# Optimization experiments

Hardware: AMD Instinct MI355X
Metric: run time of the kernel (lower is better)

## Reference

```python
import jax, jax.numpy as jnp
import numpy as np

EMBED_DIM = 1024
NUM_HEADS = 16
HEAD_DIM = EMBED_DIM // NUM_HEADS


def setup_inputs() -> dict:
    key = jax.random.key(0)
    ks = jax.random.split(key, 9)
    B, S, D = 1, 4096, EMBED_DIM
    scale = 1.0 / np.sqrt(D)
    x = jax.random.normal(ks[0], (B, S, D), dtype=jnp.float32)
    # Linear weights stored as [in, out]; torch nn.Linear init ~ U(-1/sqrt(in), 1/sqrt(in))
    wq = jax.random.uniform(ks[1], (D, D), jnp.float32, -scale, scale)
    bq = jax.random.uniform(ks[2], (D,), jnp.float32, -scale, scale)
    wk = jax.random.uniform(ks[3], (D, D), jnp.float32, -scale, scale)
    bk = jax.random.uniform(ks[4], (D,), jnp.float32, -scale, scale)
    wv = jax.random.uniform(ks[5], (D, D), jnp.float32, -scale, scale)
    bv = jax.random.uniform(ks[6], (D,), jnp.float32, -scale, scale)
    wo = jax.random.uniform(ks[7], (D, D), jnp.float32, -scale, scale)
    bo = jax.random.uniform(ks[8], (D,), jnp.float32, -scale, scale)
    return {"x": x, "wq": wq, "bq": bq, "wk": wk, "bk": bk,
            "wv": wv, "bv": bv, "wo": wo, "bo": bo}


def reference(x, wq, bq, wk, bk, wv, bv, wo, bo):
    B, S, D = x.shape
    H, Hd = NUM_HEADS, HEAD_DIM
    # QKV projections
    q = x @ wq + bq  # [B,S,D]
    k = x @ wk + bk
    v = x @ wv + bv
    # split heads -> [B,H,S,Hd]
    q = q.reshape(B, S, H, Hd).transpose(0, 2, 1, 3)
    k = k.reshape(B, S, H, Hd).transpose(0, 2, 1, 3)
    v = v.reshape(B, S, H, Hd).transpose(0, 2, 1, 3)
    inv_sqrt_d = 1.0 / np.sqrt(Hd).astype(np.float32)
    scores = jnp.einsum('bhqd,bhkd->bhqk', q, k) * inv_sqrt_d  # [B,H,S,S]
    attn = jax.nn.softmax(scores, axis=-1)
    out = jnp.einsum('bhqk,bhkd->bhqd', attn, v)  # [B,H,S,Hd]
    out = out.transpose(0, 2, 1, 3).reshape(B, S, D)
    return out @ wo + bo
```

## Files before the change

kernel.cpp:

```cpp
#include <hip/hip_runtime.h>

typedef unsigned short u16;
typedef unsigned int u32;
typedef short v8s __attribute__((ext_vector_type(8)));
typedef float f32x4 __attribute__((ext_vector_type(4)));
typedef float f32x16 __attribute__((ext_vector_type(16)));

#define S_LEN 4096
#define DM 1024
#define HDIM 64
#define CEXP 0.18033688f

__device__ __forceinline__ u16 f2bs(float f) {
  u32 u = __float_as_uint(f);
  u32 r = 0x7FFFu + ((u >> 16) & 1u);
  return (u16)((u + r) >> 16);
}

__device__ __forceinline__ float fexp2(float x) {
  float r;
  asm("v_exp_f32 %0, %1" : "=v"(r) : "v"(x));
  return r;
}

__device__ __forceinline__ void gstage16(const void* g, void* lds_wave_base) {
  __builtin_amdgcn_global_load_lds(
      (const __attribute__((address_space(1))) u32*)g,
      (__attribute__((address_space(3))) u32*)lds_wave_base, 16, 0, 0);
}

__device__ __forceinline__ f32x16 vzero16() {
  f32x16 v;
#pragma unroll
  for (int r = 0; r < 16; ++r) v[r] = 0.f;
  return v;
}

__global__ void k_cvt(const float* __restrict__ in, u16* __restrict__ out) {
  const int i = blockIdx.x * blockDim.x + threadIdx.x;
  const float4* p = reinterpret_cast<const float4*>(in) + (size_t)i * 2;
  float4 a = p[0], b = p[1];
  u16 t[8] = {f2bs(a.x), f2bs(a.y), f2bs(a.z), f2bs(a.w),
              f2bs(b.x), f2bs(b.y), f2bs(b.z), f2bs(b.w)};
  reinterpret_cast<uint4*>(out)[i] = *reinterpret_cast<const uint4*>(t);
}

__global__ __launch_bounds__(256) void k_wtrans(
    const float* __restrict__ w0, const float* __restrict__ w1,
    const float* __restrict__ w2, const float* __restrict__ w3,
    u16* __restrict__ t0, u16* __restrict__ t1,
    u16* __restrict__ t2, u16* __restrict__ t3) {
  __shared__ float tile[32][33];
  const float* w; u16* wt;
  switch (blockIdx.z) {
    case 0: w = w0; wt = t0; break;
    case 1: w = w1; wt = t1; break;
    case 2: w = w2; wt = t2; break;
    default: w = w3; wt = t3; break;
  }
  const int r = threadIdx.x >> 3;
  const int c4 = (threadIdx.x & 7) * 4;
  const int k0 = blockIdx.x * 32, n0 = blockIdx.y * 32;
  float4 v = *reinterpret_cast<const float4*>(w + (size_t)(k0 + r) * DM + n0 + c4);
  tile[r][c4] = v.x; tile[r][c4 + 1] = v.y; tile[r][c4 + 2] = v.z; tile[r][c4 + 3] = v.w;
  __syncthreads();
  u16 o4[4] = {f2bs(tile[c4][r]), f2bs(tile[c4 + 1][r]),
               f2bs(tile[c4 + 2][r]), f2bs(tile[c4 + 3][r])};
  *reinterpret_cast<uint2*>(wt + (size_t)(n0 + r) * DM + k0 + c4) =
      *reinterpret_cast<const uint2*>(o4);
}

template <int MODE>
__device__ __forceinline__ void gemm_core(
    u16* __restrict__ As, u16* __restrict__ Bs,
    const u16* __restrict__ A, const u16* __restrict__ Bt,
    const float* __restrict__ bias, void* __restrict__ Cout, float oscale) {
  constexpr int K = DM, N = DM;
  const int tid = threadIdx.x;
  const int lane = tid & 63, wave = tid >> 6;
  const int wm = wave >> 1, wn = wave & 1;
  const int l15 = lane & 15, l4 = lane >> 4;
  const int bm0 = blockIdx.x * 128, bn0 = blockIdx.y * 128;

  f32x4 acc[4][4];
#pragma unroll
  for (int m = 0; m < 4; ++m)
#pragma unroll
    for (int n = 0; n < 4; ++n) acc[m][n] = 0.f;

  const int s0 = tid, s1 = tid + 256;
  const int ra0 = s0 >> 2, ca0 = ((s0 & 3) ^ ((ra0 >> 1) & 3)) * 8;
  const int ra1 = s1 >> 2, ca1 = ((s1 & 3) ^ ((ra1 >> 1) & 3)) * 8;
  const u16* Ab = A + (size_t)bm0 * K;
  const u16* Bb = Bt + (size_t)bn0 * K;
  u16* ldsA0 = As + (size_t)(wave * 64) * 8;
  u16* ldsA1 = As + (size_t)(256 + wave * 64) * 8;
  u16* ldsB0 = Bs + (size_t)(wave * 64) * 8;
  u16* ldsB1 = Bs + (size_t)(256 + wave * 64) * 8;

  for (int k0 = 0; k0 < K; k0 += 32) {
    gstage16(Ab + (size_t)ra0 * K + k0 + ca0, ldsA0);
    gstage16(Ab + (size_t)ra1 * K + k0 + ca1, ldsA1);
    gstage16(Bb + (size_t)ra0 * K + k0 + ca0, ldsB0);
    gstage16(Bb + (size_t)ra1 * K + k0 + ca1, ldsB1);
    __syncthreads();
    v8s af[4], bfr[4];
#pragma unroll
    for (int m = 0; m < 4; ++m) {
      const int rowa = wm * 64 + m * 16 + l15;
      af[m] = *reinterpret_cast<const v8s*>(
          As + (size_t)(rowa * 4 + (l4 ^ ((rowa >> 1) & 3))) * 8);
      const int rowb = wn * 64 + m * 16 + l15;
      bfr[m] = *reinterpret_cast<const v8s*>(
          Bs + (size_t)(rowb * 4 + (l4 ^ ((rowb >> 1) & 3))) * 8);
    }
#pragma unroll
    for (int m = 0; m < 4; ++m)
#pragma unroll
      for (int n = 0; n < 4; ++n)
        acc[m][n] = __builtin_amdgcn_mfma_f32_16x16x32_bf16(af[m], bfr[n], acc[m][n], 0, 0, 0);
    __syncthreads();
  }

#pragma unroll
  for (int m = 0; m < 4; ++m) {
    const int gs0 = bm0 + wm * 64 + m * 16 + l4 * 4;
#pragma unroll
    for (int n = 0; n < 4; ++n) {
      const int gn = bn0 + wn * 64 + n * 16 + l15;
      const float bv = bias[gn];
      if (MODE == 0) {
        u16* O = (u16*)Cout;
        const size_t base = (size_t)(gn >> 6) * (S_LEN * HDIM) + (size_t)(gn & 63);
#pragma unroll
        for (int r = 0; r < 4; ++r)
          O[base + (size_t)(gs0 + r) * HDIM] = f2bs((acc[m][n][r] + bv) * oscale);
      } else if (MODE == 1) {
        u16* O = (u16*)Cout;
        u16 p4[4];
#pragma unroll
        for (int r = 0; r < 4; ++r) p4[r] = f2bs(acc[m][n][r] + bv);
        *reinterpret_cast<uint2*>(O + (size_t)(gn >> 6) * (HDIM * S_LEN) +
                                  (size_t)(gn & 63) * S_LEN + gs0) =
            *reinterpret_cast<const uint2*>(p4);
      } else {
        float* O = (float*)Cout;
#pragma unroll
        for (int r = 0; r < 4; ++r)
          O[(size_t)(gs0 + r) * N + gn] = acc[m][n][r] + bv;
      }
    }
  }
}

__global__ __launch_bounds__(256) void k_gemm_qkv(
    const u16* __restrict__ A,
    const u16* __restrict__ wq, const u16* __restrict__ wk, const u16* __restrict__ wv,
    const float* __restrict__ bq, const float* __restrict__ bk, const float* __restrict__ bv,
    u16* __restrict__ Qo, u16* __restrict__ Ko, u16* __restrict__ Vo) {
  __shared__ __attribute__((aligned(16))) u16 As[128 * 32];
  __shared__ __attribute__((aligned(16))) u16 Bs[128 * 32];
  const int z = blockIdx.z;
  if (z == 0)      gemm_core<0>(As, Bs, A, wq, bq, Qo, CEXP);
  else if (z == 1) gemm_core<0>(As, Bs, A, wk, bk, Ko, 1.f);
  else             gemm_core<1>(As, Bs, A, wv, bv, Vo, 1.f);
}

__global__ __launch_bounds__(256) void k_gemm_o(
    const u16* __restrict__ A, const u16* __restrict__ wo,
    const float* __restrict__ bo, float* __restrict__ out) {
  __shared__ __attribute__((aligned(16))) u16 As[128 * 32];
  __shared__ __attribute__((aligned(16))) u16 Bs[128 * 32];
  gemm_core<2>(As, Bs, A, wo, bo, out, 1.f);
}

__global__ __launch_bounds__(256, 2) void k_attn(
    const u16* __restrict__ Q, const u16* __restrict__ Kg,
    const u16* __restrict__ Vt, u16* __restrict__ Aout) {
  __shared__ __attribute__((aligned(16))) u16 Ks[4][64 * 64];
  __shared__ __attribute__((aligned(16))) u16 Vs[4][64 * 64];

  const int tid = threadIdx.x;
  const int lane = tid & 63, wave = tid >> 6;
  const int l31 = lane & 31, lh = lane >> 5;

  const int id = blockIdx.x;
  const int xcd = id & 7, sp = id >> 3;
  const int h = xcd * 2 + (sp & 1);
  const int qb = sp >> 1;
  const int q0 = qb * 128 + wave * 32;

  const u16* Qh = Q + (size_t)h * S_LEN * HDIM;
  const u16* Kh = Kg + (size_t)h * S_LEN * HDIM;
  const u16* Vh = Vt + (size_t)h * HDIM * S_LEN;

  v8s qf[4];
#pragma unroll
  for (int ks = 0; ks < 4; ++ks)
    qf[ks] = *reinterpret_cast<const v8s*>(
        Qh + (size_t)(q0 + l31) * HDIM + ks * 16 + lh * 8);

  const short ONE = 0x3F80;
  const v8s ones = {ONE, ONE, ONE, ONE, ONE, ONE, ONE, ONE};
  const f32x16 z16 = vzero16();

  f32x16 oacc[2], accl;
  oacc[0] = z16; oacc[1] = z16; accl = z16;

  const int s0i = tid, s1i = tid + 256;
  const int r0 = s0i >> 3, c0 = ((s0i & 7) ^ (r0 & 7)) * 8;
  const int r1 = s1i >> 3, c1 = ((s1i & 7) ^ (r1 & 7)) * 8;

  auto stageKV = [&](int b, int t) {
    const int kv0 = t * 64;
    gstage16(Kh + (size_t)(kv0 + r0) * HDIM + c0, &Ks[b][(wave * 64) * 8]);
    gstage16(Kh + (size_t)(kv0 + r1) * HDIM + c1, &Ks[b][(256 + wave * 64) * 8]);
    gstage16(Vh + (size_t)r0 * S_LEN + kv0 + c0, &Vs[b][(wave * 64) * 8]);
    gstage16(Vh + (size_t)r1 * S_LEN + kv0 + c1, &Vs[b][(256 + wave * 64) * 8]);
  };

  auto qk = [&](const u16* Kb, f32x16 (&sO)[2]) {
    __builtin_amdgcn_s_setprio(1);
#pragma unroll
    for (int j = 0; j < 2; ++j) {
      const int row = j * 32 + l31;
      v8s k0 = *reinterpret_cast<const v8s*>(
          Kb + (size_t)(row * 8 + ((0 + lh) ^ (row & 7))) * 8);
      sO[j] = __builtin_amdgcn_mfma_f32_32x32x16_bf16(k0, qf[0], z16, 0, 0, 0);
#pragma unroll
      for (int ks = 1; ks < 4; ++ks) {
        v8s kf = *reinterpret_cast<const v8s*>(
            Kb + (size_t)(row * 8 + ((ks * 2 + lh) ^ (row & 7))) * 8);
        sO[j] = __builtin_amdgcn_mfma_f32_32x32x16_bf16(kf, qf[ks], sO[j], 0, 0, 0);
      }
    }
    __builtin_amdgcn_s_setprio(0);
  };

  auto halfTile = [&](const u16* Vb, f32x16 (&sIn)[2]) {
    v8s vf[2][4];
#pragma unroll
    for (int n = 0; n < 2; ++n) {
      const int row = n * 32 + l31;
#pragma unroll
      for (int ks = 0; ks < 4; ++ks)
        vf[n][ks] = *reinterpret_cast<const v8s*>(
            Vb + (size_t)(row * 8 + ((ks * 2 + lh) ^ (row & 7))) * 8);
    }

    v8s pf[4];
#pragma unroll
    for (int jj = 0; jj < 2; ++jj) {
      float p[16];
#pragma unroll
      for (int r = 0; r < 16; ++r) p[r] = fexp2(sIn[jj][r]);
      u32 X1, X2, X3, X4, Y1, Y2, Y3, Y4;
      asm("v_cvt_pk_bf16_f32 %0, %1, %2" : "=v"(X1) : "v"(p[0]), "v"(p[1]));
      asm("v_cvt_pk_bf16_f32 %0, %1, %2" : "=v"(Y1) : "v"(p[4]), "v"(p[5]));
      asm("v_cvt_pk_bf16_f32 %0, %1, %2" : "=v"(X2) : "v"(p[2]), "v"(p[3]));
      asm("v_cvt_pk_bf16_f32 %0, %1, %2" : "=v"(Y2) : "v"(p[6]), "v"(p[7]));
      asm("v_cvt_pk_bf16_f32 %0, %1, %2" : "=v"(X3) : "v"(p[8]), "v"(p[9]));
      asm("v_cvt_pk_bf16_f32 %0, %1, %2" : "=v"(Y3) : "v"(p[12]), "v"(p[13]));
      asm("v_cvt_pk_bf16_f32 %0, %1, %2" : "=v"(X4) : "v"(p[10]), "v"(p[11]));
      asm("v_cvt_pk_bf16_f32 %0, %1, %2" : "=v"(Y4) : "v"(p[14]), "v"(p[15]));
      asm("v_permlane32_swap_b32 %0, %1" : "+v"(X1), "+v"(Y1));
      asm("v_permlane32_swap_b32 %0, %1" : "+v"(X2), "+v"(Y2));
      asm("v_permlane32_swap_b32 %0, %1" : "+v"(X3), "+v"(Y3));
      asm("v_permlane32_swap_b32 %0, %1" : "+v"(X4), "+v"(Y4));
      uint4 w0; w0.x = X1; w0.y = X2; w0.z = Y1; w0.w = Y2;
      uint4 w1; w1.x = X3; w1.y = X4; w1.z = Y3; w1.w = Y4;
      pf[jj * 2 + 0] = *reinterpret_cast<const v8s*>(&w0);
      pf[jj * 2 + 1] = *reinterpret_cast<const v8s*>(&w1);
    }

    __builtin_amdgcn_s_setprio(1);
#pragma unroll
    for (int ks = 0; ks < 4; ++ks) {
      accl = __builtin_amdgcn_mfma_f32_32x32x16_bf16(pf[ks], ones, accl, 0, 0, 0);
      oacc[0] = __builtin_amdgcn_mfma_f32_32x32x16_bf16(pf[ks], vf[0][ks], oacc[0], 0, 0, 0);
      oacc[1] = __builtin_amdgcn_mfma_f32_32x32x16_bf16(pf[ks], vf[1][ks], oacc[1], 0, 0, 0);
    }
    __builtin_amdgcn_s_setprio(0);
  };

  f32x16 sacc0[2], sacc1[2];

  auto body2 = [&](int t, int b0, int b1, int b2, int b3, bool doStage) {
    asm volatile("s_waitcnt vmcnt(0)\n\ts_barrier" ::: "memory");
    if (doStage) { stageKV(b2, t + 2); stageKV(b3, t + 3); }
    qk(&Ks[b0][0], sacc0);
    qk(&Ks[b1][0], sacc1);
    halfTile(&Vs[b0][0], sacc0);
    halfTile(&Vs[b1][0], sacc1);
  };

  stageKV(0, 0);
  stageKV(1, 1);

  for (int tt = 0; tt < 60; tt += 4) {
    body2(tt, 0, 1, 2, 3, true);
    body2(tt + 2, 2, 3, 0, 1, true);
  }
  body2(60, 0, 1, 2, 3, true);
  body2(62, 2, 3, 0, 1, false);

#pragma unroll
  for (int r = 0; r < 16; ++r) {
    const float inv = __builtin_amdgcn_rcpf(accl[r]);
    const int q = q0 + (r & 3) + 8 * (r >> 2) + 4 * lh;
    const size_t base = (size_t)q * DM + h * HDIM + l31;
    Aout[base] = f2bs(oacc[0][r] * inv);
    Aout[base + 32] = f2bs(oacc[1][r] * inv);
  }
}

extern "C" void kernel_launch(void* const* d_in, const int* in_sizes, int n_in,
                              void* d_out, int out_size, void* d_ws, size_t ws_size,
                              hipStream_t stream) {
  const float* x  = (const float*)d_in[0];
  const float* wq = (const float*)d_in[1];
  const float* bq = (const float*)d_in[2];
  const float* wk = (const float*)d_in[3];
  const float* bk = (const float*)d_in[4];
  const float* wv = (const float*)d_in[5];
  const float* bv = (const float*)d_in[6];
  const float* wo = (const float*)d_in[7];
  const float* bo = (const float*)d_in[8];
  float* out = (float*)d_out;

  char* ws = (char*)d_ws;
  u16* xb  = (u16*)(ws);
  u16* wqT = (u16*)(ws + (8u << 20));
  u16* wkT = wqT + 1024 * 1024;
  u16* wvT = wkT + 1024 * 1024;
  u16* woT = wvT + 1024 * 1024;
  u16* Qh  = (u16*)(ws + (16u << 20));
  u16* Kh  = Qh + 16 * 4096 * 64;
  u16* Vth = Kh + 16 * 4096 * 64;
  u16* Ao  = Vth + 16 * 4096 * 64;

  k_cvt<<<2048, 256, 0, stream>>>(x, xb);
  dim3 tg(32, 32, 4);
  k_wtrans<<<tg, 256, 0, stream>>>(wq, wk, wv, wo, wqT, wkT, wvT, woT);
  dim3 gg(32, 8, 3);
  k_gemm_qkv<<<gg, 256, 0, stream>>>(xb, wqT, wkT, wvT, bq, bk, bv, Qh, Kh, Vth);
  k_attn<<<512, 256, 0, stream>>>(Qh, Kh, Vth, Ao);
  dim3 og(32, 8);
  k_gemm_o<<<og, 256, 0, stream>>>(Ao, woT, bo, out);
}
```

Measured before the change: 159.6 us.

## Merge prep kernels, narrow output GEMM tiles, compute softmax sum with VALU adds

Merges the x conversion and weight transpose into one launch, removing a kernel launch. The output projection gets its own kernel with 128x64 tiles, doubling the block count to fill more compute units. In attention, the row-sum MFMA against a ones matrix is replaced by scalar adds of the exponentials plus a lane swap and shuffle at the end, freeing a third of the PV-stage matrix-core work at the cost of extra VALU adds.

Result: faster. 153.3 us (-4.0%).

```diff
diff --git a/kernel.cpp b/kernel.cpp
--- a/kernel.cpp
+++ b/kernel.cpp
@@ -36,38 +36,41 @@
   return v;
 }
 
-__global__ void k_cvt(const float* __restrict__ in, u16* __restrict__ out) {
-  const int i = blockIdx.x * blockDim.x + threadIdx.x;
-  const float4* p = reinterpret_cast<const float4*>(in) + (size_t)i * 2;
-  float4 a = p[0], b = p[1];
-  u16 t[8] = {f2bs(a.x), f2bs(a.y), f2bs(a.z), f2bs(a.w),
-              f2bs(b.x), f2bs(b.y), f2bs(b.z), f2bs(b.w)};
-  reinterpret_cast<uint4*>(out)[i] = *reinterpret_cast<const uint4*>(t);
-}
-
-__global__ __launch_bounds__(256) void k_wtrans(
+__global__ __launch_bounds__(256) void k_prep(
+    const float* __restrict__ x,
     const float* __restrict__ w0, const float* __restrict__ w1,
     const float* __restrict__ w2, const float* __restrict__ w3,
+    u16* __restrict__ xb,
     u16* __restrict__ t0, u16* __restrict__ t1,
     u16* __restrict__ t2, u16* __restrict__ t3) {
-  __shared__ float tile[32][33];
-  const float* w; u16* wt;
-  switch (blockIdx.z) {
-    case 0: w = w0; wt = t0; break;
-    case 1: w = w1; wt = t1; break;
-    case 2: w = w2; wt = t2; break;
-    default: w = w3; wt = t3; break;
-  }
-  const int r = threadIdx.x >> 3;
-  const int c4 = (threadIdx.x & 7) * 4;
-  const int k0 = blockIdx.x * 32, n0 = blockIdx.y * 32;
-  float4 v = *reinterpret_cast<const float4*>(w + (size_t)(k0 + r) * DM + n0 + c4);
-  tile[r][c4] = v.x; tile[r][c4 + 1] = v.y; tile[r][c4 + 2] = v.z; tile[r][c4 + 3] = v.w;
-  __syncthreads();
-  u16 o4[4] = {f2bs(tile[c4][r]), f2bs(tile[c4 + 1][r]),
-               f2bs(tile[c4 + 2][r]), f2bs(tile[c4 + 3][r])};
-  *reinterpret_cast<uint2*>(wt + (size_t)(n0 + r) * DM + k0 + c4) =
-      *reinterpret_cast<const uint2*>(o4);
+  const int z = blockIdx.z;
+  if (z < 4) {
+    __shared__ float tile[32][33];
+    const float* w; u16* wt;
+    switch (z) {
+      case 0: w = w0; wt = t0; break;
+      case 1: w = w1; wt = t1; break;
+      case 2: w = w2; wt = t2; break;
+      default: w = w3; wt = t3; break;
+    }
+    const int r = threadIdx.x >> 3;
+    const int c4 = (threadIdx.x & 7) * 4;
+    const int k0 = blockIdx.x * 32, n0 = blockIdx.y * 32;
+    float4 v = *reinterpret_cast<const float4*>(w + (size_t)(k0 + r) * DM + n0 + c4);
+    tile[r][c4] = v.x; tile[r][c4 + 1] = v.y; tile[r][c4 + 2] = v.z; tile[r][c4 + 3] = v.w;
+    __syncthreads();
+    u16 o4[4] = {f2bs(tile[c4][r]), f2bs(tile[c4 + 1][r]),
+                 f2bs(tile[c4 + 2][r]), f2bs(tile[c4 + 3][r])};
+    *reinterpret_cast<uint2*>(wt + (size_t)(n0 + r) * DM + k0 + c4) =
+        *reinterpret_cast<const uint2*>(o4);
+  } else {
+    const int ci = ((z - 4) * 1024 + blockIdx.y * 32 + blockIdx.x) * 256 + threadIdx.x;
+    const float4* p = reinterpret_cast<const float4*>(x) + (size_t)ci * 2;
+    float4 a = p[0], b = p[1];
+    u16 t[8] = {f2bs(a.x), f2bs(a.y), f2bs(a.z), f2bs(a.w),
+                f2bs(b.x), f2bs(b.y), f2bs(b.z), f2bs(b.w)};
+    reinterpret_cast<uint4*>(xb)[ci] = *reinterpret_cast<const uint4*>(t);
+  }
 }
 
 template <int MODE>
@@ -75,7 +78,7 @@
     u16* __restrict__ As, u16* __restrict__ Bs,
     const u16* __restrict__ A, const u16* __restrict__ Bt,
     const float* __restrict__ bias, void* __restrict__ Cout, float oscale) {
-  constexpr int K = DM, N = DM;
+  constexpr int K = DM;
   const int tid = threadIdx.x;
   const int lane = tid & 63, wave = tid >> 6;
   const int wm = wave >> 1, wn = wave & 1;
@@ -135,7 +138,7 @@
 #pragma unroll
         for (int r = 0; r < 4; ++r)
           O[base + (size_t)(gs0 + r) * HDIM] = f2bs((acc[m][n][r] + bv) * oscale);
-      } else if (MODE == 1) {
+      } else {
         u16* O = (u16*)Cout;
         u16 p4[4];
 #pragma unroll
@@ -143,11 +146,6 @@
         *reinterpret_cast<uint2*>(O + (size_t)(gn >> 6) * (HDIM * S_LEN) +
                                   (size_t)(gn & 63) * S_LEN + gs0) =
             *reinterpret_cast<const uint2*>(p4);
-      } else {
-        float* O = (float*)Cout;
-#pragma unroll
-        for (int r = 0; r < 4; ++r)
-          O[(size_t)(gs0 + r) * N + gn] = acc[m][n][r] + bv;
       }
     }
   }
@@ -170,8 +168,68 @@
     const u16* __restrict__ A, const u16* __restrict__ wo,
     const float* __restrict__ bo, float* __restrict__ out) {
   __shared__ __attribute__((aligned(16))) u16 As[128 * 32];
-  __shared__ __attribute__((aligned(16))) u16 Bs[128 * 32];
-  gemm_core<2>(As, Bs, A, wo, bo, out, 1.f);
+  __shared__ __attribute__((aligned(16))) u16 Bs[64 * 32];
+  constexpr int K = DM, N = DM;
+  const int tid = threadIdx.x;
+  const int lane = tid & 63, wave = tid >> 6;
+  const int wm = wave >> 1, wn = wave & 1;
+  const int l15 = lane & 15, l4 = lane >> 4;
+  const int bm0 = blockIdx.x * 128, bn0 = blockIdx.y * 64;
+
+  f32x4 acc[4][2];
+#pragma unroll
+  for (int m = 0; m < 4; ++m)
+#pragma unroll
+    for (int n = 0; n < 2; ++n) acc[m][n] = 0.f;
+
+  const int s0 = tid, s1 = tid + 256;
+  const int ra0 = s0 >> 2, ca0 = ((s0 & 3) ^ ((ra0 >> 1) & 3)) * 8;
+  const int ra1 = s1 >> 2, ca1 = ((s1 & 3) ^ ((ra1 >> 1) & 3)) * 8;
+  const int rb = tid >> 2,  cb = ((tid & 3) ^ ((rb >> 1) & 3)) * 8;
+  const u16* Ab = A + (size_t)bm0 * K;
+  const u16* Bb = wo + (size_t)bn0 * K;
+  u16* ldsA0 = As + (size_t)(wave * 64) * 8;
+  u16* ldsA1 = As + (size_t)(256 + wave * 64) * 8;
+  u16* ldsB0 = Bs + (size_t)(wave * 64) * 8;
+
+  for (int k0 = 0; k0 < K; k0 += 32) {
+    gstage16(Ab + (size_t)ra0 * K + k0 + ca0, ldsA0);
+    gstage16(Ab + (size_t)ra1 * K + k0 + ca1, ldsA1);
+    gstage16(Bb + (size_t)rb * K + k0 + cb, ldsB0);
+    __syncthreads();
+    v8s af[4], bfr[2];
+#pragma unroll
+    for (int m = 0; m < 4; ++m) {
+      const int rowa = wm * 64 + m * 16 + l15;
+      af[m] = *reinterpret_cast<const v8s*>(
+          As + (size_t)(rowa * 4 + (l4 ^ ((rowa >> 1) & 3))) * 8);
+    }
+#pragma unroll
+    for (int n = 0; n < 2; ++n) {
+      const int rowb = wn * 32 + n * 16 + l15;
+      bfr[n] = *reinterpret_cast<const v8s*>(
+          Bs + (size_t)(rowb * 4 + (l4 ^ ((rowb >> 1) & 3))) * 8);
+    }
+#pragma unroll
+    for (int m = 0; m < 4; ++m)
+#pragma unroll
+      for (int n = 0; n < 2; ++n)
+        acc[m][n] = __builtin_amdgcn_mfma_f32_16x16x32_bf16(af[m], bfr[n], acc[m][n], 0, 0, 0);
+    __syncthreads();
+  }
+
+#pragma unroll
+  for (int m = 0; m < 4; ++m) {
+    const int gs0 = bm0 + wm * 64 + m * 16 + l4 * 4;
+#pragma unroll
+    for (int n = 0; n < 2; ++n) {
+      const int gn = bn0 + wn * 32 + n * 16 + l15;
+      const float bv = bo[gn];
+#pragma unroll
+      for (int r = 0; r < 4; ++r)
+        out[(size_t)(gs0 + r) * N + gn] = acc[m][n][r] + bv;
+    }
+  }
 }
 
 __global__ __launch_bounds__(256, 2) void k_attn(
@@ -200,12 +258,10 @@
     qf[ks] = *reinterpret_cast<const v8s*>(
         Qh + (size_t)(q0 + l31) * HDIM + ks * 16 + lh * 8);
 
-  const short ONE = 0x3F80;
-  const v8s ones = {ONE, ONE, ONE, ONE, ONE, ONE, ONE, ONE};
   const f32x16 z16 = vzero16();
-
-  f32x16 oacc[2], accl;
-  oacc[0] = z16; oacc[1] = z16; accl = z16;
+  f32x16 oacc[2];
+  oacc[0] = z16; oacc[1] = z16;
+  float lsum = 0.f;
 
   const int s0i = tid, s1i = tid + 256;
   const int r0 = s0i >> 3, c0 = ((s0i & 7) ^ (r0 & 7)) * 8;
@@ -254,6 +310,8 @@
       float p[16];
 #pragma unroll
       for (int r = 0; r < 16; ++r) p[r] = fexp2(sIn[jj][r]);
+      lsum += ((p[0] + p[1]) + (p[2] + p[3])) + ((p[4] + p[5]) + (p[6] + p[7])) +
+              (((p[8] + p[9]) + (p[10] + p[11])) + ((p[12] + p[13]) + (p[14] + p[15])));
       u32 X1, X2, X3, X4, Y1, Y2, Y3, Y4;
       asm("v_cvt_pk_bf16_f32 %0, %1, %2" : "=v"(X1) : "v"(p[0]), "v"(p[1]));
       asm("v_cvt_pk_bf16_f32 %0, %1, %2" : "=v"(Y1) : "v"(p[4]), "v"(p[5]));
@@ -276,7 +334,6 @@
     __builtin_amdgcn_s_setprio(1);
 #pragma unroll
     for (int ks = 0; ks < 4; ++ks) {
-      accl = __builtin_amdgcn_mfma_f32_32x32x16_bf16(pf[ks], ones, accl, 0, 0, 0);
       oacc[0] = __builtin_amdgcn_mfma_f32_32x32x16_bf16(pf[ks], vf[0][ks], oacc[0], 0, 0, 0);
       oacc[1] = __builtin_amdgcn_mfma_f32_32x32x16_bf16(pf[ks], vf[1][ks], oacc[1], 0, 0, 0);
     }
@@ -304,10 +361,15 @@
   body2(60, 0, 1, 2, 3, true);
   body2(62, 2, 3, 0, 1, false);
 
+  u32 ua = __float_as_uint(lsum), ub = ua;
+  asm("v_permlane32_swap_b32 %0, %1" : "+v"(ua), "+v"(ub));
+  const float lf = __uint_as_float(ua) + __uint_as_float(ub);
+
 #pragma unroll
   for (int r = 0; r < 16; ++r) {
-    const float inv = __builtin_amdgcn_rcpf(accl[r]);
-    const int q = q0 + (r & 3) + 8 * (r >> 2) + 4 * lh;
+    const int crow = (r & 3) + 8 * (r >> 2) + 4 * lh;
+    const float inv = __builtin_amdgcn_rcpf(__shfl(lf, crow));
+    const int q = q0 + crow;
     const size_t base = (size_t)q * DM + h * HDIM + l31;
     Aout[base] = f2bs(oacc[0][r] * inv);
     Aout[base + 32] = f2bs(oacc[1][r] * inv);
@@ -339,12 +401,11 @@
   u16* Vth = Kh + 16 * 4096 * 64;
   u16* Ao  = Vth + 16 * 4096 * 64;
 
-  k_cvt<<<2048, 256, 0, stream>>>(x, xb);
-  dim3 tg(32, 32, 4);
-  k_wtrans<<<tg, 256, 0, stream>>>(wq, wk, wv, wo, wqT, wkT, wvT, woT);
+  dim3 pg(32, 32, 6);
+  k_prep<<<pg, 256, 0, stream>>>(x, wq, wk, wv, wo, xb, wqT, wkT, wvT, woT);
   dim3 gg(32, 8, 3);
   k_gemm_qkv<<<gg, 256, 0, stream>>>(xb, wqT, wkT, wvT, bq, bk, bv, Qh, Kh, Vth);
   k_attn<<<512, 256, 0, stream>>>(Qh, Kh, Vth, Ao);
-  dim3 og(32, 8);
+  dim3 og(32, 16);
   k_gemm_o<<<og, 256, 0, stream>>>(Ao, woT, bo, out);
 }
```
